# Performance work log

Hardware: AMD Instinct MI355X
Metric: run time of the kernel (lower is better)

## Reference

```python
import jax, jax.numpy as jnp
import numpy as np
from jax import lax

SEQ_LEN = 131072
EMBED_DIM = 256
DT = 0.1
EPS = 1e-8


def setup_inputs() -> dict:
    key = jax.random.key(0)
    k1, k2, k3, k4 = jax.random.split(key, 4)
    psi_real = jax.random.normal(k1, (SEQ_LEN, EMBED_DIM), dtype=jnp.float32)
    psi_imag = jax.random.normal(k2, (SEQ_LEN, EMBED_DIM), dtype=jnp.float32)
    # Hermitian Hamiltonian: H = (A + A^H)/2 with A ~ 0.1*randn (complex)
    a_re = jax.random.normal(k3, (EMBED_DIM, EMBED_DIM), dtype=jnp.float32) * 0.1
    a_im = jax.random.normal(k4, (EMBED_DIM, EMBED_DIM), dtype=jnp.float32) * 0.1
    ham_real = (a_re + a_re.T) / 2.0   # symmetric real part
    ham_imag = (a_im - a_im.T) / 2.0   # antisymmetric imag part
    hbar = jnp.ones((1,), dtype=jnp.float32)
    return {"psi_real": psi_real, "psi_imag": psi_imag,
            "ham_real": ham_real, "ham_imag": ham_imag,
            "hbar": hbar, "time_steps": 10}


def reference(psi_real, psi_imag, ham_real, ham_imag, hbar, time_steps):
    psi = psi_real + 1j * psi_imag                      # [S, D] complex64
    H = ham_real + 1j * ham_imag                        # [D, D] complex64
    coef = (-1j / hbar[0].astype(jnp.complex64)) * DT   # scalar complex

    def step(p, _):
        h_psi = p @ H.T                                 # [S, D] complex matmul
        p = p + coef * h_psi                            # Schrodinger Euler step
        norms = jnp.sqrt(jnp.sum(p.real * p.real + p.imag * p.imag,
                                 axis=1, keepdims=True))  # torch.norm over dim=1
        return p / (norms + EPS), None

    psi_out, _ = lax.scan(step, psi, None, length=time_steps)
    return psi_out
```

## Files before the change

### kernel.cpp

```cpp
#include <hip/hip_runtime.h>

#define SEQ 131072
#define DIM 256
#define DTC 0.1f
#define EPSC 1e-8f

typedef __attribute__((ext_vector_type(8))) short bf16x8;
typedef __attribute__((ext_vector_type(4))) float f32x4;
typedef __attribute__((ext_vector_type(4))) int   i32x4;

static __device__ __forceinline__ unsigned short f2bf(float f){
  unsigned int u = __builtin_bit_cast(unsigned int, f);
  u += 0x7fffu + ((u >> 16) & 1u);
  return (unsigned short)(u >> 16);
}

__global__ __launch_bounds__(1024)
void k_chain1(const float* __restrict__ hr, const float* __restrict__ hi,
              const float* __restrict__ hbar, const int* __restrict__ ts,
              float* __restrict__ m1r, float* __restrict__ m1i,
              float* __restrict__ outr, float* __restrict__ outi)
{
  __shared__ float rowr[256], rowi[256];
  __shared__ float pr_[4][256], pi_[4][256];
  const int tid = threadIdx.x, c = tid & 255, q = tid >> 8;
  const int r = blockIdx.x;
  const float s = DTC / hbar[0];
  const int T = ts[0];
  const bool b4 = ((T >> 4) & 1) != 0;
  const bool b3 = ((T >> 3) & 1) != 0;

  float m1rc = 0.f, m1ic = 0.f;
  if (q == 0){
    const int idx = r*256 + c;
    const float diag = (r == c) ? 1.0f : 0.0f;
    m1rc = diag + s * hi[idx];
    m1ic =       -s * hr[idx];
    m1r[idx] = m1rc;  m1i[idx] = m1ic;
  }

  if (!b4){
    if (q == 0){
      const float diag = (r == c) ? 1.0f : 0.0f;
      outr[r*256+c] = b3 ? m1rc : diag;
      outi[r*256+c] = b3 ? m1ic : 0.0f;
    }
    return;
  }

  if (q == 0){ rowr[c] = m1rc; rowi[c] = m1ic; }
  __syncthreads();
  float ar = 0.f, ai = 0.f;
  const int k0 = q * 64;
  #pragma unroll 4
  for (int k = k0; k < k0 + 64; ++k){
    const int idx = k*256 + c;
    const float diag = (k == c) ? 1.0f : 0.0f;
    const float br = diag + s * hi[idx];
    const float bi =       -s * hr[idx];
    const float xr = rowr[k], xi = rowi[k];
    ar = fmaf(xr, br, fmaf(-xi, bi, ar));
    ai = fmaf(xr, bi, fmaf( xi, br, ai));
  }
  pr_[q][c] = ar; pi_[q][c] = ai;
  __syncthreads();

  if (!b3){
    if (q == 0){
      outr[r*256+c] = pr_[0][c]+pr_[1][c]+pr_[2][c]+pr_[3][c];
      outi[r*256+c] = pi_[0][c]+pi_[1][c]+pi_[2][c]+pi_[3][c];
    }
    return;
  }
  if (q == 0){
    rowr[c] = pr_[0][c]+pr_[1][c]+pr_[2][c]+pr_[3][c];
    rowi[c] = pi_[0][c]+pi_[1][c]+pi_[2][c]+pi_[3][c];
  }
  __syncthreads();
  ar = 0.f; ai = 0.f;
  #pragma unroll 4
  for (int k = k0; k < k0 + 64; ++k){
    const int idx = k*256 + c;
    const float diag = (k == c) ? 1.0f : 0.0f;
    const float br = diag + s * hi[idx];
    const float bi =       -s * hr[idx];
    const float xr = rowr[k], xi = rowi[k];
    ar = fmaf(xr, br, fmaf(-xi, bi, ar));
    ai = fmaf(xr, bi, fmaf( xi, br, ai));
  }
  pr_[q][c] = ar; pi_[q][c] = ai;
  __syncthreads();
  if (q == 0){
    outr[r*256+c] = pr_[0][c]+pr_[1][c]+pr_[2][c]+pr_[3][c];
    outi[r*256+c] = pi_[0][c]+pi_[1][c]+pi_[2][c]+pi_[3][c];
  }
}

template<int BIT>
__global__ __launch_bounds__(1024)
void k_step2(const float* __restrict__ inr, const float* __restrict__ ini,
             const float* __restrict__ m1r, const float* __restrict__ m1i,
             const int* __restrict__ ts,
             float* __restrict__ outr, float* __restrict__ outi)
{
  __shared__ float rr[256], ri[256];
  __shared__ float pr_[4][256], pi_[4][256];
  const int tid = threadIdx.x, c = tid & 255, q = tid >> 8;
  const int r = blockIdx.x;
  if (q == 0){ rr[c] = inr[r*256 + c]; ri[c] = ini[r*256 + c]; }
  __syncthreads();

  float ar = 0.f, ai = 0.f;
  const int k0 = q * 64;
  #pragma unroll 8
  for (int k = k0; k < k0 + 64; ++k){
    const float br = inr[k*256 + c], bi = ini[k*256 + c];
    const float xr = rr[k],          xi = ri[k];
    ar = fmaf(xr, br, fmaf(-xi, bi, ar));
    ai = fmaf(xr, bi, fmaf( xi, br, ai));
  }
  pr_[q][c] = ar; pi_[q][c] = ai;
  __syncthreads();

  const bool bit = ((ts[0] >> BIT) & 1) != 0;
  if (!bit){
    if (q == 0){
      outr[r*256+c] = pr_[0][c]+pr_[1][c]+pr_[2][c]+pr_[3][c];
      outi[r*256+c] = pi_[0][c]+pi_[1][c]+pi_[2][c]+pi_[3][c];
    }
    return;
  }
  if (q == 0){
    rr[c] = pr_[0][c]+pr_[1][c]+pr_[2][c]+pr_[3][c];
    ri[c] = pi_[0][c]+pi_[1][c]+pi_[2][c]+pi_[3][c];
  }
  __syncthreads();
  ar = 0.f; ai = 0.f;
  #pragma unroll 8
  for (int k = k0; k < k0 + 64; ++k){
    const float br = m1r[k*256 + c], bi = m1i[k*256 + c];
    const float xr = rr[k],          xi = ri[k];
    ar = fmaf(xr, br, fmaf(-xi, bi, ar));
    ai = fmaf(xr, bi, fmaf( xi, br, ai));
  }
  pr_[q][c] = ar; pi_[q][c] = ai;
  __syncthreads();
  if (q == 0){
    outr[r*256+c] = pr_[0][c]+pr_[1][c]+pr_[2][c]+pr_[3][c];
    outi[r*256+c] = pi_[0][c]+pi_[1][c]+pi_[2][c]+pi_[3][c];
  }
}

__global__ __launch_bounds__(1024)
void k_last2(const float* __restrict__ inr, const float* __restrict__ ini,
             const float* __restrict__ m1r, const float* __restrict__ m1i,
             const int* __restrict__ ts,
             float* __restrict__ outr, float* __restrict__ outi,
             unsigned short* __restrict__ fragbuf)
{
  __shared__ float rr[256], ri[256];
  __shared__ float pr_[4][256], pi_[4][256];
  const int tid = threadIdx.x, c = tid & 255, q = tid >> 8;
  const int r = blockIdx.x;
  if (q == 0){ rr[c] = inr[r*256 + c]; ri[c] = ini[r*256 + c]; }
  __syncthreads();

  float ar = 0.f, ai = 0.f;
  const int k0 = q * 64;
  #pragma unroll 8
  for (int k = k0; k < k0 + 64; ++k){
    const float br = inr[k*256 + c], bi = ini[k*256 + c];
    const float xr = rr[k],          xi = ri[k];
    ar = fmaf(xr, br, fmaf(-xi, bi, ar));
    ai = fmaf(xr, bi, fmaf( xi, br, ai));
  }
  pr_[q][c] = ar; pi_[q][c] = ai;
  __syncthreads();

  const bool bit = (ts[0] & 1) != 0;
  if (bit){
    if (q == 0){
      rr[c] = pr_[0][c]+pr_[1][c]+pr_[2][c]+pr_[3][c];
      ri[c] = pi_[0][c]+pi_[1][c]+pi_[2][c]+pi_[3][c];
    }
    __syncthreads();
    ar = 0.f; ai = 0.f;
    #pragma unroll 8
    for (int k = k0; k < k0 + 64; ++k){
      const float br = m1r[k*256 + c], bi = m1i[k*256 + c];
      const float xr = rr[k],          xi = ri[k];
      ar = fmaf(xr, br, fmaf(-xi, bi, ar));
      ai = fmaf(xr, bi, fmaf( xi, br, ai));
    }
    pr_[q][c] = ar; pi_[q][c] = ai;
    __syncthreads();
  }

  if (q == 0){
    const float orr = pr_[0][c]+pr_[1][c]+pr_[2][c]+pr_[3][c];
    const float oii = pi_[0][c]+pi_[1][c]+pi_[2][c]+pi_[3][c];
    outr[r*256+c] = orr;
    outi[r*256+c] = oii;
    if (fragbuf){
      const int C = r, K = c;
      const int ftid = (C>>5)*64 + ((K>>3)&3)*16 + (C&15);
      const int fid  = (((C>>4)&1)*8 + (K>>5))*2;
      fragbuf[((size_t)fid*512     + ftid)*8 + (K&7)] = f2bf(orr - ((r==c)?1.0f:0.0f));
      fragbuf[((size_t)(fid+1)*512 + ftid)*8 + (K&7)] = f2bf(oii);
    }
  }
}

template<int STORE_COMPLEX>
__global__ __launch_bounds__(512, 4)
void apply5(const float* __restrict__ psi_re, const float* __restrict__ psi_im,
            const unsigned short* __restrict__ fragbuf,
            const int* __restrict__ tsteps, float* __restrict__ out)
{
  __shared__ alignas(16) unsigned short a_re[32][272];
  __shared__ alignas(16) unsigned short a_im[32][272];
  __shared__ float partials[32][8];

  const int tid  = threadIdx.x;
  const int wv   = tid >> 6;
  const int lane = tid & 63;
  const int lq   = lane >> 4;
  const int lr   = lane & 15;
  const int brow = blockIdx.x << 5;
  const int cbase = wv << 5;
  const int T = tsteps[0];
  const bf16x8* fb = reinterpret_cast<const bf16x8*>(fragbuf);

  const int srow  = tid >> 4;
  const int scol0 = (tid & 15) << 4;
  const float4* pre4 = reinterpret_cast<const float4*>(&psi_re[(size_t)(brow + srow)*DIM + scol0]);
  const float4* pim4 = reinterpret_cast<const float4*>(&psi_im[(size_t)(brow + srow)*DIM + scol0]);
  const float4 sr0 = pre4[0], sr1 = pre4[1], sr2 = pre4[2], sr3 = pre4[3];
  const float4 si0 = pim4[0], si1 = pim4[1], si2 = pim4[2], si3 = pim4[3];

  float qre[2][2][4], qim[2][2][4];
  #pragma unroll
  for (int rt = 0; rt < 2; ++rt)
    #pragma unroll
    for (int ct = 0; ct < 2; ++ct)
      #pragma unroll
      for (int j = 0; j < 4; ++j){
        const size_t off = (size_t)(brow + rt*16 + lq*4 + j)*DIM + cbase + ct*16 + lr;
        qre[rt][ct][j] = psi_re[off];
        qim[rt][ct][j] = psi_im[off];
      }

  const bf16x8 hb_r0 = fb[( 0)*512 + tid];
  const bf16x8 hb_i0 = fb[( 1)*512 + tid];
  const bf16x8 hb_r1 = fb[(16)*512 + tid];
  const bf16x8 hb_i1 = fb[(17)*512 + tid];

  {
    bf16x8 p0, p1;
    p0[0]=(short)f2bf(sr0.x); p0[1]=(short)f2bf(sr0.y); p0[2]=(short)f2bf(sr0.z); p0[3]=(short)f2bf(sr0.w);
    p0[4]=(short)f2bf(sr1.x); p0[5]=(short)f2bf(sr1.y); p0[6]=(short)f2bf(sr1.z); p0[7]=(short)f2bf(sr1.w);
    p1[0]=(short)f2bf(sr2.x); p1[1]=(short)f2bf(sr2.y); p1[2]=(short)f2bf(sr2.z); p1[3]=(short)f2bf(sr2.w);
    p1[4]=(short)f2bf(sr3.x); p1[5]=(short)f2bf(sr3.y); p1[6]=(short)f2bf(sr3.z); p1[7]=(short)f2bf(sr3.w);
    *reinterpret_cast<bf16x8*>(&a_re[srow][scol0])     = p0;
    *reinterpret_cast<bf16x8*>(&a_re[srow][scol0 + 8]) = p1;
    bf16x8 q0, q1;
    q0[0]=(short)f2bf(si0.x); q0[1]=(short)f2bf(si0.y); q0[2]=(short)f2bf(si0.z); q0[3]=(short)f2bf(si0.w);
    q0[4]=(short)f2bf(si1.x); q0[5]=(short)f2bf(si1.y); q0[6]=(short)f2bf(si1.z); q0[7]=(short)f2bf(si1.w);
    q1[0]=(short)f2bf(si2.x); q1[1]=(short)f2bf(si2.y); q1[2]=(short)f2bf(si2.z); q1[3]=(short)f2bf(si2.w);
    q1[4]=(short)f2bf(si3.x); q1[5]=(short)f2bf(si3.y); q1[6]=(short)f2bf(si3.z); q1[7]=(short)f2bf(si3.w);
    *reinterpret_cast<bf16x8*>(&a_im[srow][scol0])     = q0;
    *reinterpret_cast<bf16x8*>(&a_im[srow][scol0 + 8]) = q1;
  }
  __syncthreads();

  f32x4 ar[2][2], ai[2][2];
  #pragma unroll
  for (int rt = 0; rt < 2; ++rt)
    #pragma unroll
    for (int ct = 0; ct < 2; ++ct){
      ar[rt][ct] = (f32x4){0.f,0.f,0.f,0.f};
      ai[rt][ct] = (f32x4){0.f,0.f,0.f,0.f};
    }

  #pragma unroll
  for (int kt = 0; kt < 8; ++kt){
    bf16x8 br0, bi0, br1, bi1;
    if (kt == 0){ br0 = hb_r0; bi0 = hb_i0; br1 = hb_r1; bi1 = hb_i1; }
    else {
      br0 = fb[((0*8 + kt)*2 + 0)*512 + tid];
      bi0 = fb[((0*8 + kt)*2 + 1)*512 + tid];
      br1 = fb[((1*8 + kt)*2 + 0)*512 + tid];
      bi1 = fb[((1*8 + kt)*2 + 1)*512 + tid];
    }
    #pragma unroll
    for (int rt = 0; rt < 2; ++rt){
      const bf16x8 apr = *reinterpret_cast<const bf16x8*>(&a_re[rt*16 + lr][kt*32 + lq*8]);
      const bf16x8 api = *reinterpret_cast<const bf16x8*>(&a_im[rt*16 + lr][kt*32 + lq*8]);
      const i32x4 tneg = __builtin_bit_cast(i32x4, api) ^ (i32x4)(int)0x80008000;
      const bf16x8 apin = __builtin_bit_cast(bf16x8, tneg);
      ar[rt][0] = __builtin_amdgcn_mfma_f32_16x16x32_bf16(apr,  br0, ar[rt][0], 0,0,0);
      ar[rt][0] = __builtin_amdgcn_mfma_f32_16x16x32_bf16(apin, bi0, ar[rt][0], 0,0,0);
      ai[rt][0] = __builtin_amdgcn_mfma_f32_16x16x32_bf16(apr,  bi0, ai[rt][0], 0,0,0);
      ai[rt][0] = __builtin_amdgcn_mfma_f32_16x16x32_bf16(api,  br0, ai[rt][0], 0,0,0);
      ar[rt][1] = __builtin_amdgcn_mfma_f32_16x16x32_bf16(apr,  br1, ar[rt][1], 0,0,0);
      ar[rt][1] = __builtin_amdgcn_mfma_f32_16x16x32_bf16(apin, bi1, ar[rt][1], 0,0,0);
      ai[rt][1] = __builtin_amdgcn_mfma_f32_16x16x32_bf16(apr,  bi1, ai[rt][1], 0,0,0);
      ai[rt][1] = __builtin_amdgcn_mfma_f32_16x16x32_bf16(api,  br1, ai[rt][1], 0,0,0);
    }
  }

  #pragma unroll
  for (int rt = 0; rt < 2; ++rt)
    #pragma unroll
    for (int j = 0; j < 4; ++j){
      qre[rt][0][j] += ar[rt][0][j];
      qim[rt][0][j] += ai[rt][0][j];
      qre[rt][1][j] += ar[rt][1][j];
      qim[rt][1][j] += ai[rt][1][j];
      float v = qre[rt][0][j]*qre[rt][0][j] + qim[rt][0][j]*qim[rt][0][j]
              + qre[rt][1][j]*qre[rt][1][j] + qim[rt][1][j]*qim[rt][1][j];
      v += __shfl_xor(v, 1);
      v += __shfl_xor(v, 2);
      v += __shfl_xor(v, 4);
      v += __shfl_xor(v, 8);
      if (lr == 0) partials[rt*16 + lq*4 + j][wv] = v;
    }
  __syncthreads();

  #pragma unroll
  for (int rt = 0; rt < 2; ++rt)
    #pragma unroll
    for (int j = 0; j < 4; ++j){
      const int rl = rt*16 + lq*4 + j;
      const f32x4 p0 = *reinterpret_cast<const f32x4*>(&partials[rl][0]);
      const f32x4 p1 = *reinterpret_cast<const f32x4*>(&partials[rl][4]);
      const float nrm = ((p0[0]+p0[1]) + (p0[2]+p0[3]))
                      + ((p1[0]+p1[1]) + (p1[2]+p1[3]));
      const float sc = (T == 0) ? 1.0f : 1.0f/(sqrtf(nrm) + EPSC);
      const size_t off = (size_t)(brow + rl)*DIM + cbase + lr;
      if (STORE_COMPLEX){
        float2 v0 = {qre[rt][0][j]*sc, qim[rt][0][j]*sc};
        float2 v1 = {qre[rt][1][j]*sc, qim[rt][1][j]*sc};
        *reinterpret_cast<float2*>(&out[off*2])      = v0;
        *reinterpret_cast<float2*>(&out[(off+16)*2]) = v1;
      } else {
        out[off]    = qre[rt][0][j]*sc;
        out[off+16] = qre[rt][1][j]*sc;
      }
    }
}

template<int STORE_COMPLEX>
__global__ __launch_bounds__(512, 2)
void apply_kernel(const float* __restrict__ psi_re, const float* __restrict__ psi_im,
                  const float* __restrict__ Pre,    const float* __restrict__ Pim,
                  const int* __restrict__ tsteps,   float* __restrict__ out)
{
  __shared__ alignas(16) unsigned short a_re[64][272];
  __shared__ alignas(16) unsigned short a_im[64][272];
  __shared__ float partials[64][8];
  __shared__ float scales[64];

  const int tid  = threadIdx.x;
  const int wv   = tid >> 6;
  const int lane = tid & 63;
  const int lq   = lane >> 4;
  const int lr   = lane & 15;
  const int brow = blockIdx.x << 6;
  const int cbase = wv << 5;
  const int T = tsteps[0];

  bf16x8 bhr[2][8], bhi[2][8];
  #pragma unroll
  for (int ct = 0; ct < 2; ++ct){
    const int c = cbase + ct*16 + lr;
    #pragma unroll
    for (int kt = 0; kt < 8; ++kt){
      const int kb = kt*32 + lq*8;
      const float4 pr0 = *reinterpret_cast<const float4*>(&Pre[c*DIM + kb]);
      const float4 pr1 = *reinterpret_cast<const float4*>(&Pre[c*DIM + kb + 4]);
      const float4 pi0 = *reinterpret_cast<const float4*>(&Pim[c*DIM + kb]);
      const float4 pi1 = *reinterpret_cast<const float4*>(&Pim[c*DIM + kb + 4]);
      const float re8[8] = {pr0.x,pr0.y,pr0.z,pr0.w, pr1.x,pr1.y,pr1.z,pr1.w};
      const float im8[8] = {pi0.x,pi0.y,pi0.z,pi0.w, pi1.x,pi1.y,pi1.z,pi1.w};
      bf16x8 vr, vi;
      #pragma unroll
      for (int i = 0; i < 8; ++i){
        const float rv = re8[i] - ((c == kb + i) ? 1.0f : 0.0f);
        vr[i] = (short)f2bf(rv);
        vi[i] = (short)f2bf(im8[i]);
      }
      bhr[ct][kt] = vr; bhi[ct][kt] = vi;
    }
  }

  float sre[4][2][4], simg[4][2][4];
  #pragma unroll
  for (int rt = 0; rt < 4; ++rt)
    #pragma unroll
    for (int ct = 0; ct < 2; ++ct)
      #pragma unroll
      for (int j = 0; j < 4; ++j){
        const int row = brow + rt*16 + lq*4 + j;
        const int col = cbase + ct*16 + lr;
        const float xr = psi_re[row*DIM + col];
        const float xi = psi_im[row*DIM + col];
        sre [rt][ct][j] = xr;
        simg[rt][ct][j] = xi;
        a_re[rt*16 + lq*4 + j][col] = f2bf(xr);
        a_im[rt*16 + lq*4 + j][col] = f2bf(xi);
      }
  __syncthreads();

  #pragma unroll
  for (int rt = 0; rt < 4; ++rt){
    f32x4 ar0 = {0.f,0.f,0.f,0.f}, ar1 = {0.f,0.f,0.f,0.f};
    f32x4 ai0 = {0.f,0.f,0.f,0.f}, ai1 = {0.f,0.f,0.f,0.f};
    #pragma unroll
    for (int kt = 0; kt < 8; ++kt){
      const int arow = rt*16 + lr;
      const int kofs = kt*32 + lq*8;
      bf16x8 apr = *reinterpret_cast<const bf16x8*>(&a_re[arow][kofs]);
      bf16x8 api = *reinterpret_cast<const bf16x8*>(&a_im[arow][kofs]);
      i32x4 tneg = __builtin_bit_cast(i32x4, api) ^ (i32x4)(int)0x80008000;
      bf16x8 apin = __builtin_bit_cast(bf16x8, tneg);
      ar0 = __builtin_amdgcn_mfma_f32_16x16x32_bf16(apr,  bhr[0][kt], ar0, 0,0,0);
      ai0 = __builtin_amdgcn_mfma_f32_16x16x32_bf16(apr,  bhi[0][kt], ai0, 0,0,0);
      ar1 = __builtin_amdgcn_mfma_f32_16x16x32_bf16(apr,  bhr[1][kt], ar1, 0,0,0);
      ai1 = __builtin_amdgcn_mfma_f32_16x16x32_bf16(apr,  bhi[1][kt], ai1, 0,0,0);
      ar0 = __builtin_amdgcn_mfma_f32_16x16x32_bf16(apin, bhi[0][kt], ar0, 0,0,0);
      ai0 = __builtin_amdgcn_mfma_f32_16x16x32_bf16(api,  bhr[0][kt], ai0, 0,0,0);
      ar1 = __builtin_amdgcn_mfma_f32_16x16x32_bf16(apin, bhi[1][kt], ar1, 0,0,0);
      ai1 = __builtin_amdgcn_mfma_f32_16x16x32_bf16(api,  bhr[1][kt], ai1, 0,0,0);
    }
    float ss[4];
    #pragma unroll
    for (int j = 0; j < 4; ++j){
      sre [rt][0][j] += ar0[j];
      simg[rt][0][j] += ai0[j];
      sre [rt][1][j] += ar1[j];
      simg[rt][1][j] += ai1[j];
      float v = sre[rt][0][j]*sre[rt][0][j] + simg[rt][0][j]*simg[rt][0][j]
              + sre[rt][1][j]*sre[rt][1][j] + simg[rt][1][j]*simg[rt][1][j];
      v += __shfl_xor(v, 1);
      v += __shfl_xor(v, 2);
      v += __shfl_xor(v, 4);
      v += __shfl_xor(v, 8);
      ss[j] = v;
    }
    if (lr == 0){
      #pragma unroll
      for (int j = 0; j < 4; ++j)
        partials[rt*16 + lq*4 + j][wv] = ss[j];
    }
  }
  __syncthreads();

  if (tid < 64){
    float acc = 0.f;
    #pragma unroll
    for (int w = 0; w < 8; ++w) acc += partials[tid][w];
    scales[tid] = (T == 0) ? 1.0f : 1.0f / (sqrtf(acc) + EPSC);
  }
  __syncthreads();

  #pragma unroll
  for (int rt = 0; rt < 4; ++rt)
    #pragma unroll
    for (int ct = 0; ct < 2; ++ct)
      #pragma unroll
      for (int j = 0; j < 4; ++j){
        const int row = brow + rt*16 + lq*4 + j;
        const int col = cbase + ct*16 + lr;
        const float sc = scales[rt*16 + lq*4 + j];
        const float xr = sre [rt][ct][j] * sc;
        const float xi = simg[rt][ct][j] * sc;
        if (STORE_COMPLEX){
          float2 v2 = {xr, xi};
          *reinterpret_cast<float2*>(&out[(size_t)(row*DIM + col)*2]) = v2;
        } else {
          out[row*DIM + col] = xr;
        }
      }
}

template<int STORE_COMPLEX>
__global__ __launch_bounds__(512, 2)
void qevolve_kernel(const float* __restrict__ psi_re, const float* __restrict__ psi_im,
                    const float* __restrict__ ham_re, const float* __restrict__ ham_im,
                    const float* __restrict__ hbar,   const int* __restrict__ tsteps,
                    float* __restrict__ out)
{
  __shared__ alignas(16) unsigned short a_re[64][272];
  __shared__ alignas(16) unsigned short a_im[64][272];
  __shared__ float partials[64][8];
  __shared__ float scales[64];

  const int tid  = threadIdx.x;
  const int wv   = tid >> 6;
  const int lane = tid & 63;
  const int lq   = lane >> 4;
  const int lr   = lane & 15;
  const int brow = blockIdx.x << 6;
  const int cbase = wv << 5;
  const float cs = DTC / hbar[0];
  const int T = tsteps[0];

  bf16x8 bhr[2][8], bhi[2][8];
  #pragma unroll
  for (int ct = 0; ct < 2; ++ct){
    const int c = cbase + ct*16 + lr;
    #pragma unroll
    for (int kt = 0; kt < 8; ++kt){
      const int kb = kt*32 + lq*8;
      bf16x8 vr, vi;
      #pragma unroll
      for (int i = 0; i < 8; ++i){
        vr[i] = (short)f2bf(ham_re[c*DIM + kb + i]);
        vi[i] = (short)f2bf(ham_im[c*DIM + kb + i]);
      }
      bhr[ct][kt] = vr; bhi[ct][kt] = vi;
    }
  }

  float sre[4][2][4], simg[4][2][4];
  #pragma unroll
  for (int rt = 0; rt < 4; ++rt)
    #pragma unroll
    for (int ct = 0; ct < 2; ++ct)
      #pragma unroll
      for (int j = 0; j < 4; ++j){
        const int row = brow + rt*16 + lq*4 + j;
        const int col = cbase + ct*16 + lr;
        sre [rt][ct][j] = psi_re[row*DIM + col];
        simg[rt][ct][j] = psi_im[row*DIM + col];
      }

  for (int s = 0; s < T; ++s){
    #pragma unroll
    for (int rt = 0; rt < 4; ++rt)
      #pragma unroll
      for (int ct = 0; ct < 2; ++ct)
        #pragma unroll
        for (int j = 0; j < 4; ++j){
          const int row = rt*16 + lq*4 + j;
          const int col = cbase + ct*16 + lr;
          a_re[row][col] = f2bf(sre [rt][ct][j]);
          a_im[row][col] = f2bf(simg[rt][ct][j]);
        }
    __syncthreads();

    #pragma unroll
    for (int rt = 0; rt < 4; ++rt){
      f32x4 ar0 = {0.f,0.f,0.f,0.f}, ar1 = {0.f,0.f,0.f,0.f};
      f32x4 ai0 = {0.f,0.f,0.f,0.f}, ai1 = {0.f,0.f,0.f,0.f};
      #pragma unroll
      for (int kt = 0; kt < 8; ++kt){
        const int arow = rt*16 + lr;
        const int kofs = kt*32 + lq*8;
        bf16x8 apr = *reinterpret_cast<const bf16x8*>(&a_re[arow][kofs]);
        bf16x8 api = *reinterpret_cast<const bf16x8*>(&a_im[arow][kofs]);
        i32x4 tneg = __builtin_bit_cast(i32x4, api) ^ (i32x4)(int)0x80008000;
        bf16x8 apin = __builtin_bit_cast(bf16x8, tneg);
        ar0 = __builtin_amdgcn_mfma_f32_16x16x32_bf16(apr,  bhr[0][kt], ar0, 0,0,0);
        ai0 = __builtin_amdgcn_mfma_f32_16x16x32_bf16(apr,  bhi[0][kt], ai0, 0,0,0);
        ar1 = __builtin_amdgcn_mfma_f32_16x16x32_bf16(apr,  bhr[1][kt], ar1, 0,0,0);
        ai1 = __builtin_amdgcn_mfma_f32_16x16x32_bf16(apr,  bhi[1][kt], ai1, 0,0,0);
        ar0 = __builtin_amdgcn_mfma_f32_16x16x32_bf16(apin, bhi[0][kt], ar0, 0,0,0);
        ai0 = __builtin_amdgcn_mfma_f32_16x16x32_bf16(api,  bhr[0][kt], ai0, 0,0,0);
        ar1 = __builtin_amdgcn_mfma_f32_16x16x32_bf16(apin, bhi[1][kt], ar1, 0,0,0);
        ai1 = __builtin_amdgcn_mfma_f32_16x16x32_bf16(api,  bhr[1][kt], ai1, 0,0,0);
      }
      float ss[4];
      #pragma unroll
      for (int j = 0; j < 4; ++j){
        sre [rt][0][j] += cs * ai0[j];
        simg[rt][0][j] -= cs * ar0[j];
        sre [rt][1][j] += cs * ai1[j];
        simg[rt][1][j] -= cs * ar1[j];
        float v = sre[rt][0][j]*sre[rt][0][j] + simg[rt][0][j]*simg[rt][0][j]
                + sre[rt][1][j]*sre[rt][1][j] + simg[rt][1][j]*simg[rt][1][j];
        v += __shfl_xor(v, 1);
        v += __shfl_xor(v, 2);
        v += __shfl_xor(v, 4);
        v += __shfl_xor(v, 8);
        ss[j] = v;
      }
      if (lr == 0){
        #pragma unroll
        for (int j = 0; j < 4; ++j)
          partials[rt*16 + lq*4 + j][wv] = ss[j];
      }
    }
    __syncthreads();

    if (tid < 64){
      float acc = 0.f;
      #pragma unroll
      for (int w = 0; w < 8; ++w) acc += partials[tid][w];
      scales[tid] = 1.0f / (sqrtf(acc) + EPSC);
    }
    __syncthreads();

    #pragma unroll
    for (int rt = 0; rt < 4; ++rt)
      #pragma unroll
      for (int j = 0; j < 4; ++j){
        const float sc = scales[rt*16 + lq*4 + j];
        sre [rt][0][j] *= sc; sre [rt][1][j] *= sc;
        simg[rt][0][j] *= sc; simg[rt][1][j] *= sc;
      }
  }

  #pragma unroll
  for (int rt = 0; rt < 4; ++rt)
    #pragma unroll
    for (int ct = 0; ct < 2; ++ct)
      #pragma unroll
      for (int j = 0; j < 4; ++j){
        const int row = brow + rt*16 + lq*4 + j;
        const int col = cbase + ct*16 + lr;
        if (STORE_COMPLEX){
          out[(size_t)(row*DIM + col)*2 + 0] = sre [rt][ct][j];
          out[(size_t)(row*DIM + col)*2 + 1] = simg[rt][ct][j];
        } else {
          out[row*DIM + col] = sre[rt][ct][j];
        }
      }
}

extern "C" void kernel_launch(void* const* d_in, const int* in_sizes, int n_in,
                              void* d_out, int out_size, void* d_ws, size_t ws_size,
                              hipStream_t stream)
{
  const float* psi_re = (const float*)d_in[0];
  const float* psi_im = (const float*)d_in[1];
  const float* ham_re = (const float*)d_in[2];
  const float* ham_im = (const float*)d_in[3];
  const float* hbar   = (const float*)d_in[4];
  const int*   tstep  = (const int*)d_in[5];
  float* out = (float*)d_out;

  const size_t NMAT    = (size_t)DIM * DIM;
  const size_t WS_MAT  = 6 * NMAT * sizeof(float);
  const size_t WS_FRAG = 2 * 8 * 2 * 512 * 16;

  const bool cplx = (out_size == 2 * SEQ * DIM);

  if (d_ws != nullptr && ws_size >= WS_MAT){
    float* w   = (float*)d_ws;
    float* m1r = w + 0*NMAT; float* m1i = w + 1*NMAT;
    float* Ar  = w + 2*NMAT; float* Ai  = w + 3*NMAT;
    float* Br  = w + 4*NMAT; float* Bi  = w + 5*NMAT;
    const bool have_frag = (ws_size >= WS_MAT + WS_FRAG);
    unsigned short* fragbuf = have_frag ? (unsigned short*)(w + 6*NMAT) : nullptr;

    k_chain1  <<<256, 1024, 0, stream>>>(ham_re, ham_im, hbar, tstep, m1r, m1i, Br, Bi);
    k_step2<2><<<256, 1024, 0, stream>>>(Br, Bi, m1r, m1i, tstep, Ar, Ai);
    k_step2<1><<<256, 1024, 0, stream>>>(Ar, Ai, m1r, m1i, tstep, Br, Bi);
    k_last2   <<<256, 1024, 0, stream>>>(Br, Bi, m1r, m1i, tstep, Ar, Ai, fragbuf);

    if (have_frag){
      dim3 grid(SEQ / 32), block(512);
      if (cplx)
        apply5<1><<<grid, block, 0, stream>>>(psi_re, psi_im, fragbuf, tstep, out);
      else
        apply5<0><<<grid, block, 0, stream>>>(psi_re, psi_im, fragbuf, tstep, out);
    } else {
      dim3 grid(SEQ / 64), block(512);
      if (cplx)
        apply_kernel<1><<<grid, block, 0, stream>>>(psi_re, psi_im, Ar, Ai, tstep, out);
      else
        apply_kernel<0><<<grid, block, 0, stream>>>(psi_re, psi_im, Ar, Ai, tstep, out);
    }
  } else {
    dim3 grid(SEQ / 64), block(512);
    if (cplx)
      qevolve_kernel<1><<<grid, block, 0, stream>>>(psi_re, psi_im, ham_re, ham_im, hbar, tstep, out);
    else
      qevolve_kernel<0><<<grid, block, 0, stream>>>(psi_re, psi_im, ham_re, ham_im, hbar, tstep, out);
  }

  (void)in_sizes; (void)n_in;
}
```

Measured before the change: 213.5 us.

## Compute matrix power row-wise in one kernel instead of squaring chain

Replaces the four-kernel binary-exponentiation chain (M1, squarings, multiplies) with a single kernel in which each block repeatedly multiplies its own row vector by M1 = I - i*s*H, rebuilding M1 on the fly from the Hamiltonian inputs. This removes three kernel launches and the intermediate workspace matrices, at the cost of T-1 sequential vector-matrix products per block instead of about log2(T) matrix products. It also shrinks the LDS row padding in the apply kernel from 272 to 264 shorts.

```diff
diff --git a/kernel.cpp b/kernel.cpp
--- a/kernel.cpp
+++ b/kernel.cpp
@@ -16,209 +16,71 @@
 }
 
 __global__ __launch_bounds__(1024)
-void k_chain1(const float* __restrict__ hr, const float* __restrict__ hi,
-              const float* __restrict__ hbar, const int* __restrict__ ts,
-              float* __restrict__ m1r, float* __restrict__ m1i,
-              float* __restrict__ outr, float* __restrict__ outi)
+void k_power(const float* __restrict__ hr, const float* __restrict__ hi,
+             const float* __restrict__ hbar, const int* __restrict__ ts,
+             float* __restrict__ Pr, float* __restrict__ Pi,
+             unsigned short* __restrict__ fragbuf)
 {
-  __shared__ float rowr[256], rowi[256];
+  __shared__ float vr_[256], vi_[256];
   __shared__ float pr_[4][256], pi_[4][256];
   const int tid = threadIdx.x, c = tid & 255, q = tid >> 8;
   const int r = blockIdx.x;
   const float s = DTC / hbar[0];
   const int T = ts[0];
-  const bool b4 = ((T >> 4) & 1) != 0;
-  const bool b3 = ((T >> 3) & 1) != 0;
-
-  float m1rc = 0.f, m1ic = 0.f;
+
   if (q == 0){
-    const int idx = r*256 + c;
     const float diag = (r == c) ? 1.0f : 0.0f;
-    m1rc = diag + s * hi[idx];
-    m1ic =       -s * hr[idx];
-    m1r[idx] = m1rc;  m1i[idx] = m1ic;
-  }
-
-  if (!b4){
-    if (q == 0){
-      const float diag = (r == c) ? 1.0f : 0.0f;
-      outr[r*256+c] = b3 ? m1rc : diag;
-      outi[r*256+c] = b3 ? m1ic : 0.0f;
-    }
-    return;
-  }
-
-  if (q == 0){ rowr[c] = m1rc; rowi[c] = m1ic; }
+    vr_[c] = diag + s * hi[r*256 + c];
+    vi_[c] =       -s * hr[r*256 + c];
+  }
   __syncthreads();
-  float ar = 0.f, ai = 0.f;
-  const int k0 = q * 64;
-  #pragma unroll 4
-  for (int k = k0; k < k0 + 64; ++k){
-    const int idx = k*256 + c;
-    const float diag = (k == c) ? 1.0f : 0.0f;
-    const float br = diag + s * hi[idx];
-    const float bi =       -s * hr[idx];
-    const float xr = rowr[k], xi = rowi[k];
-    ar = fmaf(xr, br, fmaf(-xi, bi, ar));
-    ai = fmaf(xr, bi, fmaf( xi, br, ai));
-  }
-  pr_[q][c] = ar; pi_[q][c] = ai;
-  __syncthreads();
-
-  if (!b3){
-    if (q == 0){
-      outr[r*256+c] = pr_[0][c]+pr_[1][c]+pr_[2][c]+pr_[3][c];
-      outi[r*256+c] = pi_[0][c]+pi_[1][c]+pi_[2][c]+pi_[3][c];
-    }
-    return;
-  }
-  if (q == 0){
-    rowr[c] = pr_[0][c]+pr_[1][c]+pr_[2][c]+pr_[3][c];
-    rowi[c] = pi_[0][c]+pi_[1][c]+pi_[2][c]+pi_[3][c];
-  }
-  __syncthreads();
-  ar = 0.f; ai = 0.f;
-  #pragma unroll 4
-  for (int k = k0; k < k0 + 64; ++k){
-    const int idx = k*256 + c;
-    const float diag = (k == c) ? 1.0f : 0.0f;
-    const float br = diag + s * hi[idx];
-    const float bi =       -s * hr[idx];
-    const float xr = rowr[k], xi = rowi[k];
-    ar = fmaf(xr, br, fmaf(-xi, bi, ar));
-    ai = fmaf(xr, bi, fmaf( xi, br, ai));
-  }
-  pr_[q][c] = ar; pi_[q][c] = ai;
-  __syncthreads();
-  if (q == 0){
-    outr[r*256+c] = pr_[0][c]+pr_[1][c]+pr_[2][c]+pr_[3][c];
-    outi[r*256+c] = pi_[0][c]+pi_[1][c]+pi_[2][c]+pi_[3][c];
-  }
-}
-
-template<int BIT>
-__global__ __launch_bounds__(1024)
-void k_step2(const float* __restrict__ inr, const float* __restrict__ ini,
-             const float* __restrict__ m1r, const float* __restrict__ m1i,
-             const int* __restrict__ ts,
-             float* __restrict__ outr, float* __restrict__ outi)
-{
-  __shared__ float rr[256], ri[256];
-  __shared__ float pr_[4][256], pi_[4][256];
-  const int tid = threadIdx.x, c = tid & 255, q = tid >> 8;
-  const int r = blockIdx.x;
-  if (q == 0){ rr[c] = inr[r*256 + c]; ri[c] = ini[r*256 + c]; }
-  __syncthreads();
-
-  float ar = 0.f, ai = 0.f;
-  const int k0 = q * 64;
-  #pragma unroll 8
-  for (int k = k0; k < k0 + 64; ++k){
-    const float br = inr[k*256 + c], bi = ini[k*256 + c];
-    const float xr = rr[k],          xi = ri[k];
-    ar = fmaf(xr, br, fmaf(-xi, bi, ar));
-    ai = fmaf(xr, bi, fmaf( xi, br, ai));
-  }
-  pr_[q][c] = ar; pi_[q][c] = ai;
-  __syncthreads();
-
-  const bool bit = ((ts[0] >> BIT) & 1) != 0;
-  if (!bit){
-    if (q == 0){
-      outr[r*256+c] = pr_[0][c]+pr_[1][c]+pr_[2][c]+pr_[3][c];
-      outi[r*256+c] = pi_[0][c]+pi_[1][c]+pi_[2][c]+pi_[3][c];
-    }
-    return;
-  }
-  if (q == 0){
-    rr[c] = pr_[0][c]+pr_[1][c]+pr_[2][c]+pr_[3][c];
-    ri[c] = pi_[0][c]+pi_[1][c]+pi_[2][c]+pi_[3][c];
-  }
-  __syncthreads();
-  ar = 0.f; ai = 0.f;
-  #pragma unroll 8
-  for (int k = k0; k < k0 + 64; ++k){
-    const float br = m1r[k*256 + c], bi = m1i[k*256 + c];
-    const float xr = rr[k],          xi = ri[k];
-    ar = fmaf(xr, br, fmaf(-xi, bi, ar));
-    ai = fmaf(xr, bi, fmaf( xi, br, ai));
-  }
-  pr_[q][c] = ar; pi_[q][c] = ai;
-  __syncthreads();
-  if (q == 0){
-    outr[r*256+c] = pr_[0][c]+pr_[1][c]+pr_[2][c]+pr_[3][c];
-    outi[r*256+c] = pi_[0][c]+pi_[1][c]+pi_[2][c]+pi_[3][c];
-  }
-}
-
-__global__ __launch_bounds__(1024)
-void k_last2(const float* __restrict__ inr, const float* __restrict__ ini,
-             const float* __restrict__ m1r, const float* __restrict__ m1i,
-             const int* __restrict__ ts,
-             float* __restrict__ outr, float* __restrict__ outi,
-             unsigned short* __restrict__ fragbuf)
-{
-  __shared__ float rr[256], ri[256];
-  __shared__ float pr_[4][256], pi_[4][256];
-  const int tid = threadIdx.x, c = tid & 255, q = tid >> 8;
-  const int r = blockIdx.x;
-  if (q == 0){ rr[c] = inr[r*256 + c]; ri[c] = ini[r*256 + c]; }
-  __syncthreads();
-
-  float ar = 0.f, ai = 0.f;
-  const int k0 = q * 64;
-  #pragma unroll 8
-  for (int k = k0; k < k0 + 64; ++k){
-    const float br = inr[k*256 + c], bi = ini[k*256 + c];
-    const float xr = rr[k],          xi = ri[k];
-    ar = fmaf(xr, br, fmaf(-xi, bi, ar));
-    ai = fmaf(xr, bi, fmaf( xi, br, ai));
-  }
-  pr_[q][c] = ar; pi_[q][c] = ai;
-  __syncthreads();
-
-  const bool bit = (ts[0] & 1) != 0;
-  if (bit){
-    if (q == 0){
-      rr[c] = pr_[0][c]+pr_[1][c]+pr_[2][c]+pr_[3][c];
-      ri[c] = pi_[0][c]+pi_[1][c]+pi_[2][c]+pi_[3][c];
-    }
-    __syncthreads();
-    ar = 0.f; ai = 0.f;
+
+  for (int p = 0; p < T - 1; ++p){
+    float ar = 0.f, ai = 0.f;
+    const int k0 = q * 64;
     #pragma unroll 8
     for (int k = k0; k < k0 + 64; ++k){
-      const float br = m1r[k*256 + c], bi = m1i[k*256 + c];
-      const float xr = rr[k],          xi = ri[k];
+      const int idx = k*256 + c;
+      const float diag = (k == c) ? 1.0f : 0.0f;
+      const float br = diag + s * hi[idx];
+      const float bi =       -s * hr[idx];
+      const float xr = vr_[k], xi = vi_[k];
       ar = fmaf(xr, br, fmaf(-xi, bi, ar));
       ai = fmaf(xr, bi, fmaf( xi, br, ai));
     }
     pr_[q][c] = ar; pi_[q][c] = ai;
     __syncthreads();
+    if (q == 0){
+      vr_[c] = pr_[0][c]+pr_[1][c]+pr_[2][c]+pr_[3][c];
+      vi_[c] = pi_[0][c]+pi_[1][c]+pi_[2][c]+pi_[3][c];
+    }
+    __syncthreads();
   }
 
   if (q == 0){
-    const float orr = pr_[0][c]+pr_[1][c]+pr_[2][c]+pr_[3][c];
-    const float oii = pi_[0][c]+pi_[1][c]+pi_[2][c]+pi_[3][c];
-    outr[r*256+c] = orr;
-    outi[r*256+c] = oii;
+    float vr = vr_[c], vi = vi_[c];
+    if (T == 0){ vr = (r == c) ? 1.0f : 0.0f; vi = 0.0f; }
+    Pr[r*256 + c] = vr;
+    Pi[r*256 + c] = vi;
     if (fragbuf){
       const int C = r, K = c;
+      const float rr = vr - ((r == c) ? 1.0f : 0.0f);
       const int ftid = (C>>5)*64 + ((K>>3)&3)*16 + (C&15);
       const int fid  = (((C>>4)&1)*8 + (K>>5))*2;
-      fragbuf[((size_t)fid*512     + ftid)*8 + (K&7)] = f2bf(orr - ((r==c)?1.0f:0.0f));
-      fragbuf[((size_t)(fid+1)*512 + ftid)*8 + (K&7)] = f2bf(oii);
+      fragbuf[((size_t)fid*512     + ftid)*8 + (K&7)] = f2bf(rr);
+      fragbuf[((size_t)(fid+1)*512 + ftid)*8 + (K&7)] = f2bf(vi);
     }
   }
 }
 
 template<int STORE_COMPLEX>
 __global__ __launch_bounds__(512, 4)
-void apply5(const float* __restrict__ psi_re, const float* __restrict__ psi_im,
+void apply6(const float* __restrict__ psi_re, const float* __restrict__ psi_im,
             const unsigned short* __restrict__ fragbuf,
             const int* __restrict__ tsteps, float* __restrict__ out)
 {
-  __shared__ alignas(16) unsigned short a_re[32][272];
-  __shared__ alignas(16) unsigned short a_im[32][272];
+  __shared__ alignas(16) unsigned short a_re[32][264];
+  __shared__ alignas(16) unsigned short a_im[32][264];
   __shared__ float partials[32][8];
 
   const int tid  = threadIdx.x;
@@ -642,36 +504,32 @@
   float* out = (float*)d_out;
 
   const size_t NMAT    = (size_t)DIM * DIM;
-  const size_t WS_MAT  = 6 * NMAT * sizeof(float);
+  const size_t WS_MAT  = 2 * NMAT * sizeof(float);
   const size_t WS_FRAG = 2 * 8 * 2 * 512 * 16;
 
   const bool cplx = (out_size == 2 * SEQ * DIM);
 
   if (d_ws != nullptr && ws_size >= WS_MAT){
-    float* w   = (float*)d_ws;
-    float* m1r = w + 0*NMAT; float* m1i = w + 1*NMAT;
-    float* Ar  = w + 2*NMAT; float* Ai  = w + 3*NMAT;
-    float* Br  = w + 4*NMAT; float* Bi  = w + 5*NMAT;
+    float* w  = (float*)d_ws;
+    float* Pr = w + 0*NMAT;
+    float* Pi = w + 1*NMAT;
     const bool have_frag = (ws_size >= WS_MAT + WS_FRAG);
-    unsigned short* fragbuf = have_frag ? (unsigned short*)(w + 6*NMAT) : nullptr;
-
-    k_chain1  <<<256, 1024, 0, stream>>>(ham_re, ham_im, hbar, tstep, m1r, m1i, Br, Bi);
-    k_step2<2><<<256, 1024, 0, stream>>>(Br, Bi, m1r, m1i, tstep, Ar, Ai);
-    k_step2<1><<<256, 1024, 0, stream>>>(Ar, Ai, m1r, m1i, tstep, Br, Bi);
-    k_last2   <<<256, 1024, 0, stream>>>(Br, Bi, m1r, m1i, tstep, Ar, Ai, fragbuf);
+    unsigned short* fragbuf = have_frag ? (unsigned short*)(w + 2*NMAT) : nullptr;
+
+    k_power<<<256, 1024, 0, stream>>>(ham_re, ham_im, hbar, tstep, Pr, Pi, fragbuf);
 
     if (have_frag){
       dim3 grid(SEQ / 32), block(512);
       if (cplx)
-        apply5<1><<<grid, block, 0, stream>>>(psi_re, psi_im, fragbuf, tstep, out);
+        apply6<1><<<grid, block, 0, stream>>>(psi_re, psi_im, fragbuf, tstep, out);
       else
-        apply5<0><<<grid, block, 0, stream>>>(psi_re, psi_im, fragbuf, tstep, out);
+        apply6<0><<<grid, block, 0, stream>>>(psi_re, psi_im, fragbuf, tstep, out);
     } else {
       dim3 grid(SEQ / 64), block(512);
       if (cplx)
-        apply_kernel<1><<<grid, block, 0, stream>>>(psi_re, psi_im, Ar, Ai, tstep, out);
+        apply_kernel<1><<<grid, block, 0, stream>>>(psi_re, psi_im, Pr, Pi, tstep, out);
       else
-        apply_kernel<0><<<grid, block, 0, stream>>>(psi_re, psi_im, Ar, Ai, tstep, out);
+        apply_kernel<0><<<grid, block, 0, stream>>>(psi_re, psi_im, Pr, Pi, tstep, out);
     }
   } else {
     dim3 grid(SEQ / 64), block(512);
```

Result: slower. 276.4 us (+29.5%).
